# Kernel tuning notes

Hardware: AMD Instinct MI355X
Metric: run time of the kernel (lower is better)

Reference implementation:

```python
import jax, jax.numpy as jnp
import numpy as np

N_ATOMS = 2048
N_METAL = 512
BOX = (20.0, 20.0, 40.0)   # orthorhombic slab cell (A)
DL = 2.0                    # EwaldPotential dl -> k-grid half-extent per dim
SIGMA = 0.5540037           # 1/1.805132, Gaussian charge width
NMAX = tuple(int(np.ceil(L / DL)) for L in BOX)


def _kgrid():
    # integer reciprocal-lattice grid, k=0 excluded (built once at trace time)
    nx, ny, nz = NMAX
    g = np.stack(np.meshgrid(np.arange(-nx, nx + 1),
                             np.arange(-ny, ny + 1),
                             np.arange(-nz, nz + 1), indexing='ij'), -1).reshape(-1, 3)
    g = g[np.any(g != 0, axis=1)]
    return g.astype(np.float32)

_GRID = _kgrid()  # [K,3]


def ewald_field(r, q, cell):
    """Reciprocal-space Ewald potential phi_i = dE/dq_i for Gaussian-smeared charges.
    r:[N,3] q:[N,C] cell:[3,3] (rows = lattice vectors). Returns [N,C]."""
    V = jnp.abs(jnp.linalg.det(cell))
    recip = 2.0 * jnp.pi * jnp.linalg.inv(cell).T          # rows: reciprocal vectors
    k = jnp.asarray(_GRID, dtype=r.dtype) @ recip          # [K,3]
    k2 = jnp.sum(k * k, axis=-1)                           # [K]
    kfac = jnp.exp(-0.5 * SIGMA * SIGMA * k2) / k2         # exponent=1 kernel
    phase = r @ k.T                                        # [N,K]  (dominant traffic)
    c, s = jnp.cos(phase), jnp.sin(phase)
    cq = kfac[:, None] * (c.T @ q)                         # [K,C]
    sq = kfac[:, None] * (s.T @ q)
    return (4.0 * jnp.pi / V) * (c @ cq + s @ sq)          # [N,C]


def setup_inputs() -> dict:
    key = jax.random.key(0)
    k1, k2 = jax.random.split(key)
    box = jnp.asarray(BOX, dtype=jnp.float32)
    positions = jax.random.uniform(k1, (N_ATOMS, 3), dtype=jnp.float32) * box
    q = jax.random.normal(k2, (N_ATOMS, 1), dtype=jnp.float32) * 0.5
    cell = jnp.diag(box)
    # metal (Z=79) atoms occupy the first N_METAL slots; rest electrolyte (Z=8)
    atomic_numbers = jnp.concatenate([
        jnp.full((N_METAL,), 79, dtype=jnp.int32),
        jnp.full((N_ATOMS - N_METAL,), 8, dtype=jnp.int32)])
    return {"positions": positions, "q": q, "cell": cell,
            "atomic_numbers": atomic_numbers, "n_metal": N_METAL}


def reference(positions, q, cell, atomic_numbers, n_metal):
    nm = int(n_metal)  # static: metal atoms are the first nm rows
    dt = positions.dtype
    # q_all[metal] = 0
    q = q.at[:nm].set(0.0)
    # capacitance matrix S from detached coords (torch uses r.detach(), cell.detach())
    r_m = jax.lax.stop_gradient(positions[:nm])
    cell_d = jax.lax.stop_gradient(cell)
    A = ewald_field(r_m, jnp.eye(nm, dtype=dt), cell_d)     # [nm,nm] A_mat
    A_inv = jnp.linalg.inv(A)
    ones = jnp.ones((nm, 1), dtype=dt)
    Ai1 = A_inv @ ones                                       # [nm,1]
    S = A_inv - (Ai1 @ Ai1.T) / (ones.T @ Ai1)               # charge-neutral projector
    # full-system field; scaling_factor=1, external_field=None -> B_ext = 0
    f = ewald_field(positions, q, cell)                      # [N,1]
    B = -f[:nm]
    q_mw = q.at[:nm].set(S @ B)
    e_corr = jnp.zeros((1,), dtype=dt)   # scaling_factor == 1.0 branch
    e_ext = jnp.zeros((1,), dtype=dt)    # external_field is None
    return q_mw, e_corr, e_ext
```

## Files before the change

### kernel.cpp

```cpp
#include <hip/hip_runtime.h>
#include <math.h>

#define N_ATOMS 2048
#define NM      512
#define KHALF   9040
#define KPAD    9216
#define TWO_PI  6.2831853071795864769f
#define SIGMA   0.5540037f
#define FOUR_PI 12.566370614359172954f

__device__ inline void inv3x3(const float* __restrict__ c, float inv[3][3], float& det) {
    float a00=c[0],a01=c[1],a02=c[2],a10=c[3],a11=c[4],a12=c[5],a20=c[6],a21=c[7],a22=c[8];
    float c00 =  a11*a22 - a12*a21;
    float c01 = -(a10*a22 - a12*a20);
    float c02 =  a10*a21 - a11*a20;
    det = a00*c00 + a01*c01 + a02*c02;
    float id = 1.0f/det;
    inv[0][0] = c00*id;
    inv[0][1] = -(a01*a22 - a02*a21)*id;
    inv[0][2] =  (a01*a12 - a02*a11)*id;
    inv[1][0] = c01*id;
    inv[1][1] =  (a00*a22 - a02*a20)*id;
    inv[1][2] = -(a00*a12 - a02*a10)*id;
    inv[2][0] = c02*id;
    inv[2][1] = -(a00*a21 - a01*a20)*id;
    inv[2][2] =  (a00*a11 - a01*a10)*id;
}

__device__ __forceinline__ void gbar(int* cnt, int* flag, int ph, int G) {
    __syncthreads();
    if (threadIdx.x == 0) {
        int prev = __hip_atomic_fetch_add(cnt, 1, __ATOMIC_RELEASE, __HIP_MEMORY_SCOPE_AGENT);
        if (prev == G*ph - 1) {
            (void)__hip_atomic_load(cnt, __ATOMIC_ACQUIRE, __HIP_MEMORY_SCOPE_AGENT);
            __hip_atomic_store(flag, ph, __ATOMIC_RELEASE, __HIP_MEMORY_SCOPE_AGENT);
        } else {
            while (__hip_atomic_load(flag, __ATOMIC_RELAXED, __HIP_MEMORY_SCOPE_AGENT) < ph)
                __builtin_amdgcn_s_sleep(2);
            (void)__hip_atomic_load(flag, __ATOMIC_ACQUIRE, __HIP_MEMORY_SCOPE_AGENT);
        }
    }
    __syncthreads();
}

__global__ void prep(const float* __restrict__ pos, const float* __restrict__ qv,
                     const float* __restrict__ cell, float4* __restrict__ kdata,
                     float4* __restrict__ uq, float* __restrict__ out) {
    const int bb = blockIdx.x, tid = threadIdx.x;
    if (bb < 36) {
        int t = bb*256 + tid;
        float gx=0.f, gy=0.f, gz=0.f, wk=0.f;
        if (t < KHALF) {
            int iz = t % 41; int rem = t / 41; int iy = rem % 21; int ix = rem / 21;
            gx = (float)(ix - 10); gy = (float)(iy - 10); gz = (float)(iz - 20);
            float inv[3][3], det;
            inv3x3(cell, inv, det);
            float kx = TWO_PI*(gx*inv[0][0] + gy*inv[0][1] + gz*inv[0][2]);
            float ky = TWO_PI*(gx*inv[1][0] + gy*inv[1][1] + gz*inv[1][2]);
            float kz = TWO_PI*(gx*inv[2][0] + gy*inv[2][1] + gz*inv[2][2]);
            float k2 = kx*kx + ky*ky + kz*kz;
            float kfac = __expf(-0.5f*SIGMA*SIGMA*k2) / k2;
            wk = sqrtf(2.0f*kfac);
        }
        kdata[t] = make_float4(gx, gy, gz, wk);
    } else {
        int i = (bb-36)*256 + tid;
        float inv[3][3], det;
        inv3x3(cell, inv, det);
        float x = pos[3*i], y = pos[3*i+1], z = pos[3*i+2];
        float u = x*inv[0][0] + y*inv[1][0] + z*inv[2][0];
        float v = x*inv[0][1] + y*inv[1][1] + z*inv[2][1];
        float w = x*inv[0][2] + y*inv[1][2] + z*inv[2][2];
        float qi = qv[i];
        uq[i] = make_float4(u, v, w, qi);
        if (i >= NM) out[i] = qi;
        if (i == 0) { out[N_ATOMS] = 0.f; out[N_ATOMS+1] = 0.f; }
    }
}

__global__ void __launch_bounds__(256, 2) syrk_sf(const float4* __restrict__ kdata,
        const float4* __restrict__ uq, float* __restrict__ partial,
        float* __restrict__ Scw, float* __restrict__ Ssw, int SL, int KSL, int nsyrk) {
    __shared__ float smem[16384];
    const int tid = threadIdx.x;
    if ((int)blockIdx.x >= nsyrk) {
        int ch = blockIdx.x - nsyrk;
        int kk = tid & 63, sp = tid >> 6;
        int k = ch*64 + kk;
        float4 kd = kdata[k];
        float sc = 0.f, ss = 0.f;
        int jlo = NM + sp*384, jhi = jlo + 384;
        for (int j = jlo; j < jhi; ++j) {
            float4 at = uq[j];
            float ph = TWO_PI*(kd.x*at.x + kd.y*at.y + kd.z*at.z);
            float s, c; __sincosf(ph, &s, &c);
            sc += at.w * c;
            ss += at.w * s;
        }
        smem[sp*64 + kk] = sc;
        smem[256 + sp*64 + kk] = ss;
        __syncthreads();
        if (sp == 0) {
            float c = smem[kk] + smem[64+kk] + smem[128+kk] + smem[192+kk];
            float s = smem[256+kk] + smem[320+kk] + smem[384+kk] + smem[448+kk];
            float kf2 = kd.w * kd.w;
            Scw[k] = kf2 * c;
            Ssw[k] = kf2 * s;
        }
        return;
    }
    int s = blockIdx.x % SL;
    int t = blockIdx.x / SL;
    int rt = 0;
    while ((rt+1)*(rt+2)/2 <= t) ++rt;
    int ct = t - rt*(rt+1)/2;
    const int row0 = rt << 7, c0 = ct << 7;
    const bool diag = (row0 == c0);
    float* crT = smem; float* srT = smem+4096; float* ccT = smem+8192; float* scT = smem+12288;
    const float* ccR = diag ? crT : ccT;
    const float* scR = diag ? srT : scT;
    const int i0 = (tid & 15) << 2;
    const int j0 = (tid >> 4) << 2;
    float acc[8][8];
    #pragma unroll
    for (int i = 0; i < 8; ++i)
        #pragma unroll
        for (int j = 0; j < 8; ++j) acc[i][j] = 0.f;
    const int k0 = s * KSL;
    const int nch = KSL >> 5;
    for (int ch = 0; ch < nch; ++ch) {
        int kc = k0 + (ch << 5);
        __syncthreads();
        #pragma unroll
        for (int w = 0; w < 16; ++w) {
            int job = tid + (w << 8);
            int kk = job >> 7, a = job & 127;
            float4 kd = kdata[kc + kk];
            float4 at = uq[row0 + a];
            float ph = TWO_PI*(kd.x*at.x + kd.y*at.y + kd.z*at.z);
            float sn, cs;
            __sincosf(ph, &sn, &cs);
            crT[kk*128+a] = kd.w * cs;
            srT[kk*128+a] = kd.w * sn;
        }
        if (!diag) {
            #pragma unroll
            for (int w = 0; w < 16; ++w) {
                int job = tid + (w << 8);
                int kk = job >> 7, a = job & 127;
                float4 kd = kdata[kc + kk];
                float4 at = uq[c0 + a];
                float ph = TWO_PI*(kd.x*at.x + kd.y*at.y + kd.z*at.z);
                float sn, cs;
                __sincosf(ph, &sn, &cs);
                ccT[kk*128+a] = kd.w * cs;
                scT[kk*128+a] = kd.w * sn;
            }
        }
        __syncthreads();
        #pragma unroll 4
        for (int kk = 0; kk < 32; ++kk) {
            float4 c0v = *(const float4*)&crT[kk*128+i0];
            float4 c1v = *(const float4*)&crT[kk*128+i0+64];
            float4 s0v = *(const float4*)&srT[kk*128+i0];
            float4 s1v = *(const float4*)&srT[kk*128+i0+64];
            float4 d0v = *(const float4*)&ccR[kk*128+j0];
            float4 d1v = *(const float4*)&ccR[kk*128+j0+64];
            float4 t0v = *(const float4*)&scR[kk*128+j0];
            float4 t1v = *(const float4*)&scR[kk*128+j0+64];
            float cr[8] = {c0v.x,c0v.y,c0v.z,c0v.w, c1v.x,c1v.y,c1v.z,c1v.w};
            float sr[8] = {s0v.x,s0v.y,s0v.z,s0v.w, s1v.x,s1v.y,s1v.z,s1v.w};
            float cc[8] = {d0v.x,d0v.y,d0v.z,d0v.w, d1v.x,d1v.y,d1v.z,d1v.w};
            float sv[8] = {t0v.x,t0v.y,t0v.z,t0v.w, t1v.x,t1v.y,t1v.z,t1v.w};
            #pragma unroll
            for (int i = 0; i < 8; ++i)
                #pragma unroll
                for (int j = 0; j < 8; ++j)
                    acc[i][j] += cr[i]*cc[j] + sr[i]*sv[j];
        }
    }
    float* P = partial + ((size_t)blockIdx.x << 14);
    #pragma unroll
    for (int i = 0; i < 8; ++i) {
        int row = (i < 4) ? (i0 + i) : (64 + i0 + i - 4);
        *(float4*)&P[row*128 + j0]      = make_float4(acc[i][0], acc[i][1], acc[i][2], acc[i][3]);
        *(float4*)&P[row*128 + j0 + 64] = make_float4(acc[i][4], acc[i][5], acc[i][6], acc[i][7]);
    }
}

__device__ void diag_fast(float* D, float* T, float* M, int tid, int pd, float* Dinvs) {
    __syncthreads();
    if (tid < 64) {
        float row[64];
        #pragma unroll
        for (int c = 0; c < 64; ++c) row[c] = D[tid*68 + c];
        #pragma unroll
        for (int j = 0; j < 64; ++j) {
            float pj = __shfl(row[j], j);
            float rinv = 1.0f / sqrtf(pj);
            float lj = row[j] * rinv;
            row[j] = lj;
            #pragma unroll
            for (int c = j+1; c < 64; ++c) {
                float lcj = __shfl(lj, c);
                row[c] = fmaf(-lj, lcj, row[c]);
            }
        }
        #pragma unroll
        for (int c = 0; c < 64; ++c) D[tid*68 + c] = row[c];
    }
    __syncthreads();
    for (int idx = tid; idx < 64*68; idx += 256) T[idx] = 0.f;
    __syncthreads();
    if (tid < 64) {
        int s = tid >> 3, c = tid & 7, o = s*8;
        float x[8];
        #pragma unroll
        for (int r = 0; r < 8; ++r) {
            float acc = (r == c) ? 1.0f : 0.0f;
            #pragma unroll
            for (int j = 0; j < 8; ++j)
                if (j < r) acc -= D[(o+r)*68 + o + j] * x[j];
            x[r] = (r >= c) ? acc / D[(o+r)*68 + o + r] : 0.0f;
        }
        #pragma unroll
        for (int r = 0; r < 8; ++r)
            if (r >= c) T[(o+r)*68 + o + c] = x[r];
    }
    __syncthreads();
    #pragma unroll
    for (int lvl = 0; lvl < 3; ++lvl) {
        const int h = 8 << lvl, pairs = 4 >> lvl;
        const int hq = h >> 2, nq = pairs * h * hq;
        for (int e = tid; e < nq; e += 256) {
            int pr = e / (h*hq); int rem = e - pr*h*hq;
            int r2 = rem / hq, cq = rem - (rem/hq)*hq;
            int o = pr*2*h;
            float4 acc = make_float4(0.f, 0.f, 0.f, 0.f);
            for (int j2 = cq*4; j2 < h; ++j2) {
                float l = D[(o+h+r2)*68 + o + j2];
                float4 w = *(const float4*)&T[(o+j2)*68 + o + cq*4];
                acc.x += l*w.x; acc.y += l*w.y; acc.z += l*w.z; acc.w += l*w.w;
            }
            *(float4*)&M[(pr*h + r2)*h + cq*4] = acc;
        }
        __syncthreads();
        for (int e = tid; e < nq; e += 256) {
            int pr = e / (h*hq); int rem = e - pr*h*hq;
            int r2 = rem / hq, cq = rem - (rem/hq)*hq;
            int o = pr*2*h;
            float4 acc = make_float4(0.f, 0.f, 0.f, 0.f);
            for (int j2 = 0; j2 <= r2; ++j2) {
                float w = T[(o+h+r2)*68 + o+h + j2];
                float4 m = *(const float4*)&M[(pr*h + j2)*h + cq*4];
                acc.x += w*m.x; acc.y += w*m.y; acc.z += w*m.z; acc.w += w*m.w;
            }
            float4 st = make_float4(-acc.x, -acc.y, -acc.z, -acc.w);
            *(float4*)&T[(o+h+r2)*68 + o + cq*4] = st;
        }
        __syncthreads();
    }
    for (int idx = tid; idx < 4096; idx += 256) {
        int r = idx >> 6, c = idx & 63;
        Dinvs[pd*4096 + idx] = (c <= r) ? T[r*68+c] : 0.f;
    }
}

__global__ void __launch_bounds__(256) redfield(const float* __restrict__ partial,
        const float* __restrict__ cell, float* __restrict__ Amat,
        const float4* __restrict__ kdata, const float4* __restrict__ uq,
        const float* __restrict__ Scw, const float* __restrict__ Ssw,
        float* __restrict__ Bvec, int SL) {
    const int b = blockIdx.x, tid = threadIdx.x;
    float inv[3][3], det;
    inv3x3(cell, inv, det);
    const float scal = FOUR_PI / fabsf(det);
    if (b < 512) {
        for (int idx = b*256 + tid; idx < 512*512; idx += 512*256) {
            int i = idx >> 9, j = idx & 511;
            if (i < j) continue;
            int rt2 = i >> 7, ct2 = j >> 7;
            int t2 = rt2*(rt2+1)/2 + ct2;
            const float* p = partial + ((size_t)(t2*SL) << 14) + ((i & 127) << 7) + (j & 127);
            float a0=0.f,a1=0.f,a2=0.f,a3=0.f,a4=0.f,a5=0.f,a6=0.f,a7=0.f;
            int s = 0;
            for (; s + 8 <= SL; s += 8) {
                a0 += p[(size_t)(s+0) << 14];
                a1 += p[(size_t)(s+1) << 14];
                a2 += p[(size_t)(s+2) << 14];
                a3 += p[(size_t)(s+3) << 14];
                a4 += p[(size_t)(s+4) << 14];
                a5 += p[(size_t)(s+5) << 14];
                a6 += p[(size_t)(s+6) << 14];
                a7 += p[(size_t)(s+7) << 14];
            }
            for (; s < SL; ++s) a0 += p[(size_t)s << 14];
            float sum = ((a0+a1)+(a2+a3)) + ((a4+a5)+(a6+a7));
            float v = scal * sum;
            Amat[(size_t)i*512 + j] = v;
            Amat[(size_t)j*512 + i] = v;
        }
    } else {
        int ch = b - 512;
        int atom = ch*4 + (tid >> 6);
        int lane = tid & 63;
        float4 at = uq[atom];
        float acc = 0.f;
        for (int k = lane; k < KPAD; k += 64) {
            float4 kd = kdata[k];
            float ph = TWO_PI*(kd.x*at.x + kd.y*at.y + kd.z*at.z);
            float s, c; __sincosf(ph, &s, &c);
            acc += c*Scw[k] + s*Ssw[k];
        }
        #pragma unroll
        for (int off = 32; off; off >>= 1) acc += __shfl_down(acc, off);
        if (lane == 0) Bvec[atom] = -scal * acc;
    }
}

__device__ void chol_tile(float* Amat, float* Lmat, float* LmatT, float* Dinvs,
                          float* smem, int tid, int p, int tt) {
    int rt = 0; while ((rt+1)*(rt+2)/2 <= tt) ++rt;
    const int ct = tt - rt*(rt+1)/2;
    const int R = p + 1 + rt, C = p + 1 + ct;
    float* ArT = smem;
    float* DvT = smem + 4352;
    float* LrT = smem + 8704;
    float* LcT = smem + 13056;
    float4 pref4[4];
    if (R != C) {
        #pragma unroll
        for (int w = 0; w < 4; ++w) {
            int j = tid + (w << 8);
            pref4[w] = *(const float4*)&Amat[(size_t)(C*64 + (j >> 4))*512 + p*64 + (j & 15)*4];
        }
    }
    __syncthreads();
    #pragma unroll
    for (int w = 0; w < 4; ++w) {
        int t4 = tid + (w << 8);
        float4 v = *(const float4*)&Dinvs[p*4096 + t4*4];
        int j = t4 >> 4, d0 = (t4 & 15)*4;
        DvT[(d0+0)*68 + j] = v.x;
        DvT[(d0+1)*68 + j] = v.y;
        DvT[(d0+2)*68 + j] = v.z;
        DvT[(d0+3)*68 + j] = v.w;
    }
    #pragma unroll
    for (int w = 0; w < 4; ++w) {
        int j = tid + (w << 8);
        int i = j >> 4, k0 = (j & 15)*4;
        float4 v = *(const float4*)&Amat[(size_t)(R*64 + i)*512 + p*64 + k0];
        ArT[(k0+0)*68 + i] = v.x;
        ArT[(k0+1)*68 + i] = v.y;
        ArT[(k0+2)*68 + i] = v.z;
        ArT[(k0+3)*68 + i] = v.w;
    }
    __syncthreads();
    const int i0 = (tid & 15)*4, j0 = (tid >> 4)*4;
    float lr[4][4];
    #pragma unroll
    for (int ii = 0; ii < 4; ++ii)
        #pragma unroll
        for (int jj = 0; jj < 4; ++jj) lr[ii][jj] = 0.f;
    for (int k = 0; k < 64; ++k) {
        float4 av = *(float4*)&ArT[k*68 + i0];
        float4 dv = *(float4*)&DvT[k*68 + j0];
        lr[0][0] += av.x*dv.x; lr[0][1] += av.x*dv.y; lr[0][2] += av.x*dv.z; lr[0][3] += av.x*dv.w;
        lr[1][0] += av.y*dv.x; lr[1][1] += av.y*dv.y; lr[1][2] += av.y*dv.z; lr[1][3] += av.y*dv.w;
        lr[2][0] += av.z*dv.x; lr[2][1] += av.z*dv.y; lr[2][2] += av.z*dv.z; lr[2][3] += av.z*dv.w;
        lr[3][0] += av.w*dv.x; lr[3][1] += av.w*dv.y; lr[3][2] += av.w*dv.z; lr[3][3] += av.w*dv.w;
    }
    #pragma unroll
    for (int ii = 0; ii < 4; ++ii)
        #pragma unroll
        for (int jj = 0; jj < 4; ++jj)
            LrT[(j0+jj)*68 + i0+ii] = lr[ii][jj];
    __syncthreads();
    if (C == p + 1) {
        for (int idx = tid; idx < 4096; idx += 256) {
            int i2 = idx >> 6, c2 = idx & 63;
            Lmat[(size_t)(R*64+i2)*512 + p*64 + c2] = LrT[c2*68 + i2];
        }
        for (int idx = tid; idx < 4096; idx += 256) {
            int c2 = idx >> 6, i2 = idx & 63;
            LmatT[(size_t)(p*64+c2)*512 + R*64 + i2] = LrT[c2*68 + i2];
        }
    }
    if (R == C) {
        float up[4][4];
        #pragma unroll
        for (int ii = 0; ii < 4; ++ii)
            #pragma unroll
            for (int jj = 0; jj < 4; ++jj) up[ii][jj] = 0.f;
        for (int k = 0; k < 64; ++k) {
            float4 av = *(float4*)&LrT[k*68 + i0];
            float4 bv = *(float4*)&LrT[k*68 + j0];
            up[0][0] += av.x*bv.x; up[0][1] += av.x*bv.y; up[0][2] += av.x*bv.z; up[0][3] += av.x*bv.w;
            up[1][0] += av.y*bv.x; up[1][1] += av.y*bv.y; up[1][2] += av.y*bv.z; up[1][3] += av.y*bv.w;
            up[2][0] += av.z*bv.x; up[2][1] += av.z*bv.y; up[2][2] += av.z*bv.z; up[2][3] += av.z*bv.w;
            up[3][0] += av.w*bv.x; up[3][1] += av.w*bv.y; up[3][2] += av.w*bv.z; up[3][3] += av.w*bv.w;
        }
        float vals[4][4];
        #pragma unroll
        for (int ii = 0; ii < 4; ++ii)
            #pragma unroll
            for (int jj = 0; jj < 4; ++jj) {
                size_t gix = (size_t)(R*64+i0+ii)*512 + C*64 + j0 + jj;
                float v = Amat[gix] - up[ii][jj];
                Amat[gix] = v;
                vals[ii][jj] = v;
            }
        if (tt == 0) {
            float* D = smem; float* T = smem + 4352; float* M = smem + 8704;
            __syncthreads();
            #pragma unroll
            for (int ii = 0; ii < 4; ++ii)
                #pragma unroll
                for (int jj = 0; jj < 4; ++jj)
                    D[(i0+ii)*68 + j0+jj] = vals[ii][jj];
            diag_fast(D, T, M, tid, p+1, Dinvs);
        }
    } else {
        #pragma unroll
        for (int w = 0; w < 4; ++w) {
            int j = tid + (w << 8);
            int i = j >> 4, k0 = (j & 15)*4;
            ArT[(k0+0)*68 + i] = pref4[w].x;
            ArT[(k0+1)*68 + i] = pref4[w].y;
            ArT[(k0+2)*68 + i] = pref4[w].z;
            ArT[(k0+3)*68 + i] = pref4[w].w;
        }
        __syncthreads();
        const int c0l = (tid & 15)*4, jr0 = (tid >> 4)*2;
        #pragma unroll
        for (int hh = 0; hh < 2; ++hh) {
            float lc[4][2];
            #pragma unroll
            for (int cc = 0; cc < 4; ++cc) { lc[cc][0] = 0.f; lc[cc][1] = 0.f; }
            for (int d = 0; d < 64; ++d) {
                float4 dv = *(float4*)&DvT[d*68 + c0l];
                float2 av = *(float2*)&ArT[d*68 + hh*32 + jr0];
                lc[0][0] += dv.x*av.x; lc[0][1] += dv.x*av.y;
                lc[1][0] += dv.y*av.x; lc[1][1] += dv.y*av.y;
                lc[2][0] += dv.z*av.x; lc[2][1] += dv.z*av.y;
                lc[3][0] += dv.w*av.x; lc[3][1] += dv.w*av.y;
            }
            __syncthreads();
            #pragma unroll
            for (int cc = 0; cc < 4; ++cc) {
                LcT[(c0l+cc)*36 + jr0]     = lc[cc][0];
                LcT[(c0l+cc)*36 + jr0 + 1] = lc[cc][1];
            }
            __syncthreads();
            float up[4][2];
            #pragma unroll
            for (int ii = 0; ii < 4; ++ii) { up[ii][0] = 0.f; up[ii][1] = 0.f; }
            for (int c2 = 0; c2 < 64; ++c2) {
                float4 lv = *(float4*)&LrT[c2*68 + i0];
                float2 cv = *(float2*)&LcT[c2*36 + jr0];
                up[0][0] += lv.x*cv.x; up[0][1] += lv.x*cv.y;
                up[1][0] += lv.y*cv.x; up[1][1] += lv.y*cv.y;
                up[2][0] += lv.z*cv.x; up[2][1] += lv.z*cv.y;
                up[3][0] += lv.w*cv.x; up[3][1] += lv.w*cv.y;
            }
            #pragma unroll
            for (int ii = 0; ii < 4; ++ii)
                #pragma unroll
                for (int jr = 0; jr < 2; ++jr) {
                    size_t gix = (size_t)(R*64+i0+ii)*512 + C*64 + hh*32 + jr0 + jr;
                    Amat[gix] -= up[ii][jr];
                }
        }
    }
}

__global__ void __launch_bounds__(256) tail_chol(float* __restrict__ Amat,
        float* __restrict__ Lmat, float* __restrict__ LmatT, float* __restrict__ Dinvs,
        int* cnt, int* flag) {
    __shared__ float smem[15360];
    const int b = blockIdx.x, tid = threadIdx.x;
    const int G = 28;

    if (b == 0) {
        float* D = smem; float* T = smem + 4352; float* M = smem + 8704;
        for (int idx = tid; idx < 4096; idx += 256) {
            int r = idx >> 6, c = idx & 63;
            D[r*68+c] = Amat[(size_t)r*512 + c];
        }
        diag_fast(D, T, M, tid, 0, Dinvs);
    }
    gbar(cnt, flag, 1, G);

    for (int p = 0; p <= 3; ++p) {
        const int T7 = 7 - p, ntile = T7*(T7+1)/2;
        if (b < ntile) chol_tile(Amat, Lmat, LmatT, Dinvs, smem, tid, p, b);
        if (p < 3) gbar(cnt, flag, p + 2, G);
    }
    __syncthreads();
    if (tid == 0)
        __hip_atomic_fetch_add(cnt, 1, __ATOMIC_RELEASE, __HIP_MEMORY_SCOPE_AGENT);
    if (b != 0) return;
    if (tid == 0) {
        while (__hip_atomic_load(cnt, __ATOMIC_RELAXED, __HIP_MEMORY_SCOPE_AGENT) < G*5)
            __builtin_amdgcn_s_sleep(2);
        (void)__hip_atomic_load(cnt, __ATOMIC_ACQUIRE, __HIP_MEMORY_SCOPE_AGENT);
    }
    __syncthreads();
    for (int p = 4; p <= 6; ++p) {
        const int T7 = 7 - p, ntile = T7*(T7+1)/2;
        for (int tt = 0; tt < ntile; ++tt)
            chol_tile(Amat, Lmat, LmatT, Dinvs, smem, tid, p, tt);
    }
}

__global__ void __launch_bounds__(512) solve(const float* __restrict__ Lmat,
        const float* __restrict__ LmatT, const float* __restrict__ Dinvs,
        const float* __restrict__ Bvec, float* __restrict__ out) {
    __shared__ float smem[2592];
    float* rb  = smem;
    float* ro  = smem + 512;
    float* xb  = smem + 1024;
    float* xo  = smem + 1536;
    float* bvs = smem + 2048;
    float* red = smem + 2560;
    const int tid = threadIdx.x;
    if (tid < 512) {
        float bv = Bvec[tid];
        bvs[tid] = bv; rb[tid] = bv; ro[tid] = 1.0f;
    }
    __syncthreads();
    for (int k = 0; k < 8; ++k) {
        if (tid < 64) {
            const float* Dk = Dinvs + k*4096 + tid*64;
            float s1 = 0.f, s2 = 0.f;
            for (int c4 = 0; c4 < 16; ++c4) {
                float4 w = *(const float4*)&Dk[c4*4];
                int cb = 64*k + c4*4;
                s1 += w.x*rb[cb] + w.y*rb[cb+1] + w.z*rb[cb+2] + w.w*rb[cb+3];
                s2 += w.x*ro[cb] + w.y*ro[cb+1] + w.z*ro[cb+2] + w.w*ro[cb+3];
            }
            rb[64*k+tid] = s1; ro[64*k+tid] = s2;
        }
        __syncthreads();
        for (int mm = 64*(k+1) + tid; mm < 512; mm += 512) {
            const float* Lr = Lmat + (size_t)mm*512 + 64*k;
            float s1 = 0.f, s2 = 0.f;
            for (int c4 = 0; c4 < 16; ++c4) {
                float4 l = *(const float4*)&Lr[c4*4];
                int cb = 64*k + c4*4;
                s1 += l.x*rb[cb] + l.y*rb[cb+1] + l.z*rb[cb+2] + l.w*rb[cb+3];
                s2 += l.x*ro[cb] + l.y*ro[cb+1] + l.z*ro[cb+2] + l.w*ro[cb+3];
            }
            rb[mm] -= s1; ro[mm] -= s2;
        }
        __syncthreads();
    }
    for (int k = 7; k >= 0; --k) {
        if (tid < 64) {
            const float* D0 = Dinvs + k*4096;
            float s1 = 0.f, s2 = 0.f;
            for (int c = 0; c < 64; ++c) {
                float w = D0[c*64 + tid];
                s1 += w*rb[64*k+c]; s2 += w*ro[64*k+c];
            }
            xb[64*k+tid] = s1; xo[64*k+tid] = s2;
        }
        __syncthreads();
        for (int mm = tid; mm < 64*k; mm += 512) {
            const float* Ur = LmatT + (size_t)mm*512 + 64*k;
            float s1 = 0.f, s2 = 0.f;
            for (int c4 = 0; c4 < 16; ++c4) {
                float4 u = *(const float4*)&Ur[c4*4];
                int cb = 64*k + c4*4;
                s1 += u.x*xb[cb] + u.y*xb[cb+1] + u.z*xb[cb+2] + u.w*xb[cb+3];
                s2 += u.x*xo[cb] + u.y*xo[cb+1] + u.z*xo[cb+2] + u.w*xo[cb+3];
            }
            rb[mm] -= s1; ro[mm] -= s2;
        }
        __syncthreads();
    }
    float pn = 0.f, pd = 0.f;
    if (tid < 512) { pn = xo[tid]*bvs[tid]; pd = xo[tid]; }
    #pragma unroll
    for (int off = 32; off; off >>= 1) { pn += __shfl_down(pn, off); pd += __shfl_down(pd, off); }
    if ((tid & 63) == 0) { red[tid >> 6] = pn; red[16 + (tid >> 6)] = pd; }
    __syncthreads();
    if (tid == 0) {
        float sn = 0.f, sd = 0.f;
        #pragma unroll
        for (int i = 0; i < 8; ++i) { sn += red[i]; sd += red[16+i]; }
        red[31] = sn / sd;
    }
    __syncthreads();
    float ratio = red[31];
    if (tid < 512) out[tid] = xb[tid] - xo[tid]*ratio;
}

extern "C" void kernel_launch(void* const* d_in, const int* in_sizes, int n_in,
                              void* d_out, int out_size, void* d_ws, size_t ws_size,
                              hipStream_t stream) {
    (void)in_sizes; (void)n_in; (void)out_size;
    const float* pos  = (const float*)d_in[0];
    const float* qv   = (const float*)d_in[1];
    const float* cell = (const float*)d_in[2];
    float* out = (float*)d_out;
    char* ws = (char*)d_ws;
    size_t off = 0;
    auto alloc = [&](size_t bytes) -> void* {
        void* p = (void*)(ws + off);
        off = (off + bytes + 255) & ~(size_t)255;
        return p;
    };
    float4* kdata = (float4*)alloc((size_t)KPAD*16);
    float4* uq    = (float4*)alloc((size_t)N_ATOMS*16);
    float*  Scw   = (float*)alloc((size_t)KPAD*4);
    float*  Ssw   = (float*)alloc((size_t)KPAD*4);
    float*  Bvec  = (float*)alloc(512*4);
    float*  Amat  = (float*)alloc((size_t)512*512*4);
    float*  Lmat  = (float*)alloc((size_t)512*512*4);
    float*  LmatT = (float*)alloc((size_t)512*512*4);
    float*  Dinvs = (float*)alloc((size_t)8*4096*4);
    int* bar = (int*)alloc(256);
    static const int slopts[10] = {96, 72, 48, 36, 24, 16, 12, 8, 4, 1};
    int SL = 1;
    for (int ci = 0; ci < 10; ++ci) {
        size_t need = (size_t)10 * slopts[ci] * 16384 * 4;
        if (off + need <= ws_size) { SL = slopts[ci]; break; }
    }
    float* partial = (float*)alloc((size_t)10*SL*16384*4);
    const int KSL = KPAD / SL;
    const int nsyrk = 10*SL;

    hipMemsetAsync(bar, 0, 8, stream);
    prep<<<dim3(44), dim3(256), 0, stream>>>(pos, qv, cell, kdata, uq, out);
    syrk_sf<<<dim3(nsyrk + 144), dim3(256), 0, stream>>>(kdata, uq, partial,
                                                         Scw, Ssw, SL, KSL, nsyrk);
    redfield<<<dim3(640), dim3(256), 0, stream>>>(partial, cell, Amat, kdata, uq,
                                                  Scw, Ssw, Bvec, SL);
    tail_chol<<<dim3(28), dim3(256), 0, stream>>>(Amat, Lmat, LmatT, Dinvs,
                                                  bar, bar + 1);
    solve<<<dim3(1), dim3(512), 0, stream>>>(Lmat, LmatT, Dinvs, Bvec, out);
}
```

Measured before the change: 631.9 us.

## Pin Cholesky blocks to one XCD and run all panels with grid barriers

The Cholesky tail kernel now launches many blocks and reads the hardware XCC ID. Blocks off XCC 0 sleep before taking a ticket, so the first 28 tickets are likely claimed by blocks sharing one XCD's L2, and the extra blocks exit. Panels 4-6, which block 0 used to run serially, now go through the same grid-barrier loop spread across blocks. The syrk split-K options are also capped lower, giving fewer partials to reduce. The XCD placement relies on timing through sleeps, not a guarantee, and cross-XCD barriers are only avoided if the scheduling works out.

```diff
diff --git a/kernel.cpp b/kernel.cpp
--- a/kernel.cpp
+++ b/kernel.cpp
@@ -477,10 +477,25 @@
 
 __global__ void __launch_bounds__(256) tail_chol(float* __restrict__ Amat,
         float* __restrict__ Lmat, float* __restrict__ LmatT, float* __restrict__ Dinvs,
-        int* cnt, int* flag) {
+        int* bar) {
     __shared__ float smem[15360];
-    const int b = blockIdx.x, tid = threadIdx.x;
+    __shared__ int bslot;
+    const int tid = threadIdx.x;
     const int G = 28;
+    int* cnt = bar; int* flag = bar + 1; int* ticket = bar + 2;
+
+    if (tid == 0) {
+        int xid = 0;
+        asm volatile("s_getreg_b32 %0, hwreg(HW_REG_XCC_ID)" : "=s"(xid));
+        if ((xid & 7) != 0) {
+            #pragma unroll 1
+            for (int i = 0; i < 48; ++i) __builtin_amdgcn_s_sleep(15);
+        }
+        bslot = __hip_atomic_fetch_add(ticket, 1, __ATOMIC_RELAXED, __HIP_MEMORY_SCOPE_AGENT);
+    }
+    __syncthreads();
+    const int b = bslot;
+    if (b >= G) return;
 
     if (b == 0) {
         float* D = smem; float* T = smem + 4352; float* M = smem + 8704;
@@ -492,25 +507,10 @@
     }
     gbar(cnt, flag, 1, G);
 
-    for (int p = 0; p <= 3; ++p) {
+    for (int p = 0; p <= 6; ++p) {
         const int T7 = 7 - p, ntile = T7*(T7+1)/2;
         if (b < ntile) chol_tile(Amat, Lmat, LmatT, Dinvs, smem, tid, p, b);
-        if (p < 3) gbar(cnt, flag, p + 2, G);
-    }
-    __syncthreads();
-    if (tid == 0)
-        __hip_atomic_fetch_add(cnt, 1, __ATOMIC_RELEASE, __HIP_MEMORY_SCOPE_AGENT);
-    if (b != 0) return;
-    if (tid == 0) {
-        while (__hip_atomic_load(cnt, __ATOMIC_RELAXED, __HIP_MEMORY_SCOPE_AGENT) < G*5)
-            __builtin_amdgcn_s_sleep(2);
-        (void)__hip_atomic_load(cnt, __ATOMIC_ACQUIRE, __HIP_MEMORY_SCOPE_AGENT);
-    }
-    __syncthreads();
-    for (int p = 4; p <= 6; ++p) {
-        const int T7 = 7 - p, ntile = T7*(T7+1)/2;
-        for (int tt = 0; tt < ntile; ++tt)
-            chol_tile(Amat, Lmat, LmatT, Dinvs, smem, tid, p, tt);
+        if (p < 6) gbar(cnt, flag, p + 2, G);
     }
 }
 
@@ -622,9 +622,9 @@
     float*  LmatT = (float*)alloc((size_t)512*512*4);
     float*  Dinvs = (float*)alloc((size_t)8*4096*4);
     int* bar = (int*)alloc(256);
-    static const int slopts[10] = {96, 72, 48, 36, 24, 16, 12, 8, 4, 1};
+    static const int slopts[8] = {36, 24, 16, 12, 8, 4, 2, 1};
     int SL = 1;
-    for (int ci = 0; ci < 10; ++ci) {
+    for (int ci = 0; ci < 8; ++ci) {
         size_t need = (size_t)10 * slopts[ci] * 16384 * 4;
         if (off + need <= ws_size) { SL = slopts[ci]; break; }
     }
@@ -632,13 +632,12 @@
     const int KSL = KPAD / SL;
     const int nsyrk = 10*SL;
 
-    hipMemsetAsync(bar, 0, 8, stream);
+    hipMemsetAsync(bar, 0, 12, stream);
     prep<<<dim3(44), dim3(256), 0, stream>>>(pos, qv, cell, kdata, uq, out);
     syrk_sf<<<dim3(nsyrk + 144), dim3(256), 0, stream>>>(kdata, uq, partial,
                                                          Scw, Ssw, SL, KSL, nsyrk);
     redfield<<<dim3(640), dim3(256), 0, stream>>>(partial, cell, Amat, kdata, uq,
                                                   Scw, Ssw, Bvec, SL);
-    tail_chol<<<dim3(28), dim3(256), 0, stream>>>(Amat, Lmat, LmatT, Dinvs,
-                                                  bar, bar + 1);
+    tail_chol<<<dim3(512), dim3(256), 0, stream>>>(Amat, Lmat, LmatT, Dinvs, bar);
     solve<<<dim3(1), dim3(512), 0, stream>>>(Lmat, LmatT, Dinvs, Bvec, out);
 }
```

Result: faster. 595.6 us (-5.7%).
